# Performance work log

Measured on AMD Instinct MI355X. Metric: run time of the kernel, lower is better.

Reference implementation:

```python
import jax, jax.numpy as jnp
import numpy as np

B, D_IMG, H, V, T, EOS = 1024, 512, 512, 8192, 20, 0


def setup_inputs() -> dict:
    key = jax.random.key(0)
    ks = jax.random.split(key, 9)
    s = 1.0 / np.sqrt(H)
    return {
        "target_input": jax.random.normal(ks[0], (B, D_IMG), dtype=jnp.float32),
        "emb": jax.random.normal(ks[1], (V, H), dtype=jnp.float32),
        "fc1_w": jax.random.normal(ks[2], (H, D_IMG), dtype=jnp.float32) * (1.0 / np.sqrt(D_IMG)),
        "fc1_b": jnp.zeros((H,), jnp.float32),
        "w_ih": jax.random.normal(ks[3], (4 * H, H), dtype=jnp.float32) * s,
        "w_hh": jax.random.normal(ks[4], (4 * H, H), dtype=jnp.float32) * s,
        "b_ih": jax.random.normal(ks[5], (4 * H,), dtype=jnp.float32) * s,
        "b_hh": jax.random.normal(ks[6], (4 * H,), dtype=jnp.float32) * s,
        "out_w": jax.random.normal(ks[7], (V, H), dtype=jnp.float32) * s,
        "out_b": jnp.zeros((V,), jnp.float32),
        "max_len": T,
        "eos": EOS,
    }


def reference(target_input, emb, fc1_w, fc1_b, w_ih, w_hh, b_ih, b_hh, out_w, out_b, max_len, eos):
    Bsz = target_input.shape[0]
    Hd = w_hh.shape[1]
    # h0 = ReLU(fc1(img_latent)); c0 = 0; first token input = zeros
    h0 = jax.nn.relu(target_input @ fc1_w.T + fc1_b)
    c0 = jnp.zeros((Bsz, Hd), target_input.dtype)
    x0 = jnp.zeros((Bsz, Hd), target_input.dtype)
    mask0 = jnp.ones((Bsz,), target_input.dtype)
    keys = jax.random.split(jax.random.key(42), max_len)

    def step(carry, k):
        h, c, x, mask = carry
        # LSTMCell (PyTorch gate order i, f, g, o)
        gates = x @ w_ih.T + b_ih + h @ w_hh.T + b_hh
        i, f, g, o = jnp.split(gates, 4, axis=1)
        c = jax.nn.sigmoid(f) * c + jax.nn.sigmoid(i) * jnp.tanh(g)
        h = jax.nn.sigmoid(o) * jnp.tanh(c)
        logits = h @ out_w.T + out_b                      # [B, V]
        logp = jax.nn.log_softmax(logits, axis=-1)
        p = jnp.exp(logp)
        action = jax.random.categorical(k, logits, axis=-1)  # [B]
        lp = jnp.take_along_axis(logp, action[:, None], axis=1)[:, 0] * mask
        ent = -jnp.sum(p * logp, axis=-1) * mask
        p_masked = p * mask[:, None]
        x_next = emb[action]
        mask = mask * (1.0 - (action == eos).astype(mask.dtype))
        return (h, c, x_next, mask), (action, lp, ent, p_masked)

    _, (msgs, lps, ents, probs) = jax.lax.scan(step, (h0, c0, x0, mask0), keys)
    # scan stacks along time axis 0 -> move to axis 1
    return (msgs.T, lps.T, ents.T, jnp.transpose(probs, (1, 0, 2)))
```

## Files before the change

kernel.cpp:

```cpp
#include <hip/hip_runtime.h>
#include <math.h>

#define Bn 1024
#define Dn 512
#define Hn 512
#define Vn 8192
#define Tn 20
#define G4 2048

typedef _Float16 half8 __attribute__((ext_vector_type(8)));
typedef float f32x4 __attribute__((ext_vector_type(4)));

#define SCHEDB() __builtin_amdgcn_sched_barrier(0)
#define SBAR()   __builtin_amdgcn_s_barrier()

__host__ __device__ __forceinline__ void threefry2x32(
    unsigned k0, unsigned k1, unsigned x0, unsigned x1,
    unsigned& y0, unsigned& y1) {
  unsigned ks2 = k0 ^ k1 ^ 0x1BD11BDAu;
#define TF_RND(r) { x0 += x1; x1 = (x1 << (r)) | (x1 >> (32 - (r))); x1 ^= x0; }
  x0 += k0; x1 += k1;
  TF_RND(13) TF_RND(15) TF_RND(26) TF_RND(6)
  x0 += k1; x1 += ks2 + 1u;
  TF_RND(17) TF_RND(29) TF_RND(16) TF_RND(24)
  x0 += ks2; x1 += k0 + 2u;
  TF_RND(13) TF_RND(15) TF_RND(26) TF_RND(6)
  x0 += k0; x1 += k1 + 3u;
  TF_RND(17) TF_RND(29) TF_RND(16) TF_RND(24)
  x0 += k1; x1 += ks2 + 4u;
  TF_RND(13) TF_RND(15) TF_RND(26) TF_RND(6)
  x0 += ks2; x1 += k0 + 5u;
#undef TF_RND
  y0 = x0; y1 = x1;
}

__device__ __forceinline__ void split16(float v, _Float16& hi, _Float16& lo) {
  float h = (fabsf(v) < 6.2e-5f) ? 0.f : (float)(_Float16)v;
  hi = (_Float16)h;
  lo = (_Float16)((v - h) * 2048.0f);
}

__device__ __forceinline__ void gload16(void* l, const void* g) {
  __builtin_amdgcn_global_load_lds(
      (const __attribute__((address_space(1))) unsigned int*)g,
      (__attribute__((address_space(3))) unsigned int*)l, 16, 0, 0);
}

__global__ void k_prep(const float* __restrict__ w, _Float16* __restrict__ hi,
                       _Float16* __restrict__ lo, int n) {
  int i = blockIdx.x * blockDim.x + threadIdx.x;
  if (i >= n) return;
  split16(w[i], hi[i], lo[i]);
}

__global__ void k_prep_perm(const float* __restrict__ w, _Float16* __restrict__ hi,
                            _Float16* __restrict__ lo) {
  int i = blockIdx.x * blockDim.x + threadIdx.x;
  int rp = i >> 9, k = i & 511;
  int u = rp >> 2, g = rp & 3;
  split16(w[(size_t)((g << 9) + u) * 512 + k], hi[i], lo[i]);
}

__global__ void k_prep_bias(const float* __restrict__ bih, const float* __restrict__ bhh,
                            float* __restrict__ bp) {
  int i = blockIdx.x * blockDim.x + threadIdx.x;
  if (i >= G4) return;
  int u = i >> 2, g = i & 3;
  bp[i] = bih[(g << 9) + u] + bhh[(g << 9) + u];
}

__global__ void k_mask(float* __restrict__ mask) {
  int i = blockIdx.x * blockDim.x + threadIdx.x;
  if (i < Bn) mask[i] = 1.f;
}

__device__ __forceinline__ void cell_update(
    float (*gtile)[68], int tid, int bm, int u0, float* __restrict__ c,
    _Float16* __restrict__ hoh, _Float16* __restrict__ hol) {
#pragma unroll
  for (int j = 0; j < 8; ++j) {
    int idx = tid + (j << 8);
    int row = idx >> 4, ul = idx & 15;
    float4 gt = *(const float4*)&gtile[row][ul << 2];
    size_t cidx = (size_t)(bm + row) * Hn + u0 + ul;
    float si = 1.0f / (1.0f + expf(-gt.x));
    float sf = 1.0f / (1.0f + expf(-gt.y));
    float tg = tanhf(gt.z);
    float so = 1.0f / (1.0f + expf(-gt.w));
    float cn = sf * c[cidx] + si * tg;
    c[cidx] = cn;
    float hv = so * tanhf(cn);
    split16(hv, hoh[cidx], hol[cidx]);
  }
}

__global__ void __launch_bounds__(256) k_gates(
    const _Float16* __restrict__ xh, const _Float16* __restrict__ xl,
    const _Float16* __restrict__ hih, const _Float16* __restrict__ hil,
    const _Float16* __restrict__ wph, const _Float16* __restrict__ wpl,
    const _Float16* __restrict__ vph, const _Float16* __restrict__ vpl,
    const float* __restrict__ biasp, float* __restrict__ c,
    _Float16* __restrict__ hoh, _Float16* __restrict__ hol) {
  extern __shared__ __align__(16) char smem[];
  int tid = threadIdx.x;
  f32x4 acch[4][2] = {};
  f32x4 accc[4][2] = {};
  int x8 = blockIdx.x & 7, q = blockIdx.x >> 3;
  int bn = (((q & 3) << 3) | x8) << 6;
  int bm = (q >> 2) << 7;
  int lane = tid & 63, wv = tid >> 6;
  int wr = (wv >> 1) << 6, wc = (wv & 1) << 5;
  int fr = lane & 15, c0 = lane >> 4;
  int rsub = lane >> 2, cp = lane & 3;
  int psw = (c0 ^ ((fr >> 1) & 3)) << 3;

  auto stage = [&](int p, int t) {
    const _Float16* As_h = (t < 16) ? xh : hih;
    const _Float16* As_l = (t < 16) ? xl : hil;
    const _Float16* Bs_h = (t < 16) ? wph : vph;
    const _Float16* Bs_l = (t < 16) ? wpl : vpl;
    int k0 = (t & 15) << 5;
    char* base = smem + p * 24576;
#pragma unroll
    for (int s = 0; s < 2; ++s) {
      int row = (((wv << 1) + s) << 4) + rsub;
      int koff = (cp ^ ((row >> 1) & 3)) << 3;
      size_t ga = (size_t)(bm + row) * 512 + k0 + koff;
      int lo = (row << 5) + (cp << 3);
      gload16((_Float16*)base + lo, As_h + ga);
      gload16((_Float16*)(base + 8192) + lo, As_l + ga);
    }
    {
      int row = (wv << 4) + rsub;
      int koff = (cp ^ ((row >> 1) & 3)) << 3;
      size_t gb = (size_t)(bn + row) * 512 + k0 + koff;
      int lo = (row << 5) + (cp << 3);
      gload16((_Float16*)(base + 16384) + lo, Bs_h + gb);
      gload16((_Float16*)(base + 20480) + lo, Bs_l + gb);
    }
  };
  auto compute = [&](int p) {
    char* base = smem + p * 24576;
    _Float16 (*Ah)[32] = (_Float16(*)[32])base;
    _Float16 (*Al)[32] = (_Float16(*)[32])(base + 8192);
    _Float16 (*Bh)[32] = (_Float16(*)[32])(base + 16384);
    _Float16 (*Bl)[32] = (_Float16(*)[32])(base + 20480);
    half8 ah[4], al[4], bh[2], bl[2];
#pragma unroll
    for (int i = 0; i < 4; ++i) {
      int ra = wr + i * 16 + fr;
      ah[i] = *(const half8*)&Ah[ra][psw];
      al[i] = *(const half8*)&Al[ra][psw];
    }
#pragma unroll
    for (int i = 0; i < 2; ++i) {
      int rb = wc + i * 16 + fr;
      bh[i] = *(const half8*)&Bh[rb][psw];
      bl[i] = *(const half8*)&Bl[rb][psw];
    }
#pragma unroll
    for (int mi = 0; mi < 4; ++mi)
#pragma unroll
      for (int ni = 0; ni < 2; ++ni) {
        acch[mi][ni] = __builtin_amdgcn_mfma_f32_16x16x32_f16(ah[mi], bh[ni], acch[mi][ni], 0, 0, 0);
        accc[mi][ni] = __builtin_amdgcn_mfma_f32_16x16x32_f16(ah[mi], bl[ni], accc[mi][ni], 0, 0, 0);
        accc[mi][ni] = __builtin_amdgcn_mfma_f32_16x16x32_f16(al[mi], bh[ni], accc[mi][ni], 0, 0, 0);
      }
  };

  stage(0, 0); stage(1, 1);
  asm volatile("s_waitcnt vmcnt(6)" ::: "memory");
  SCHEDB(); SBAR(); SCHEDB();
  int pc = 0, ps = 2;
  for (int t = 0; t < 32; ++t) {
    if (t + 2 < 32) stage(ps, t + 2);
    compute(pc);
    SCHEDB();
    if (t + 2 < 32) { asm volatile("s_waitcnt vmcnt(6) lgkmcnt(0)" ::: "memory"); }
    else            { asm volatile("s_waitcnt vmcnt(0) lgkmcnt(0)" ::: "memory"); }
    SCHEDB(); SBAR(); SCHEDB();
    pc = (pc == 2) ? 0 : pc + 1;
    ps = (ps == 2) ? 0 : ps + 1;
  }

  float (*gtile)[68] = (float(*)[68])smem;
  int orow = (lane >> 4) << 2, ocol = lane & 15;
#pragma unroll
  for (int mi = 0; mi < 4; ++mi)
#pragma unroll
    for (int ni = 0; ni < 2; ++ni) {
      int col = wc + ni * 16 + ocol;
      float bsum = biasp[bn + col];
#pragma unroll
      for (int r = 0; r < 4; ++r) {
        int row = wr + mi * 16 + orow + r;
        gtile[row][col] = acch[mi][ni][r] + accc[mi][ni][r] * (1.0f / 2048.0f) + bsum;
      }
    }
  __syncthreads();
  cell_update(gtile, tid, bm, bn >> 2, c, hoh, hol);
}

__global__ void __launch_bounds__(512) k_logits(
    const _Float16* __restrict__ hh, const _Float16* __restrict__ hl,
    const _Float16* __restrict__ outwh, const _Float16* __restrict__ outwl,
    const float* __restrict__ outb, float* __restrict__ logits) {
  extern __shared__ __align__(16) char smem[];
  int tid = threadIdx.x;
  f32x4 acch[4][4] = {};
  f32x4 accc[4][4] = {};
  int x8 = blockIdx.x & 7, q = blockIdx.x >> 3;
  int bn = (((q & 7) << 3) | x8) << 7;
  int bm = (q >> 3) << 8;
  int lane = tid & 63, wv = tid >> 6;
  int wr = (wv >> 1) << 6, wc = (wv & 1) << 6;
  int fr = lane & 15, c0 = lane >> 4;
  int rsub = lane >> 2, cp = lane & 3;
  int psw = (c0 ^ ((fr >> 1) & 3)) << 3;

  auto stage = [&](int p, int t) {
    int k0 = t << 5;
    char* base = smem + p * 49152;
#pragma unroll
    for (int s = 0; s < 2; ++s) {
      int row = (((wv << 1) + s) << 4) + rsub;
      int koff = (cp ^ ((row >> 1) & 3)) << 3;
      size_t ga = (size_t)(bm + row) * 512 + k0 + koff;
      int lo = (row << 5) + (cp << 3);
      gload16((_Float16*)base + lo, hh + ga);
      gload16((_Float16*)(base + 16384) + lo, hl + ga);
    }
    {
      int row = tid >> 2;
      int koff = (cp ^ ((row >> 1) & 3)) << 3;
      size_t gb = (size_t)(bn + row) * 512 + k0 + koff;
      int lo = (row << 5) + (cp << 3);
      gload16((_Float16*)(base + 32768) + lo, outwh + gb);
      gload16((_Float16*)(base + 40960) + lo, outwl + gb);
    }
  };
  auto compute = [&](int p) {
    char* base = smem + p * 49152;
    _Float16 (*Ah)[32] = (_Float16(*)[32])base;
    _Float16 (*Al)[32] = (_Float16(*)[32])(base + 16384);
    _Float16 (*Bh)[32] = (_Float16(*)[32])(base + 32768);
    _Float16 (*Bl)[32] = (_Float16(*)[32])(base + 40960);
    half8 ah[4], al[4], bh[4], bl[4];
#pragma unroll
    for (int i = 0; i < 4; ++i) {
      int ra = wr + i * 16 + fr;
      int rb = wc + i * 16 + fr;
      ah[i] = *(const half8*)&Ah[ra][psw];
      al[i] = *(const half8*)&Al[ra][psw];
      bh[i] = *(const half8*)&Bh[rb][psw];
      bl[i] = *(const half8*)&Bl[rb][psw];
    }
#pragma unroll
    for (int mi = 0; mi < 4; ++mi)
#pragma unroll
      for (int ni = 0; ni < 4; ++ni) {
        acch[mi][ni] = __builtin_amdgcn_mfma_f32_16x16x32_f16(ah[mi], bh[ni], acch[mi][ni], 0, 0, 0);
        accc[mi][ni] = __builtin_amdgcn_mfma_f32_16x16x32_f16(ah[mi], bl[ni], accc[mi][ni], 0, 0, 0);
        accc[mi][ni] = __builtin_amdgcn_mfma_f32_16x16x32_f16(al[mi], bh[ni], accc[mi][ni], 0, 0, 0);
      }
  };

  stage(0, 0); stage(1, 1);
  asm volatile("s_waitcnt vmcnt(6)" ::: "memory");
  SCHEDB(); SBAR(); SCHEDB();
  int pc = 0, ps = 2;
  for (int t = 0; t < 16; ++t) {
    if (t + 2 < 16) stage(ps, t + 2);
    compute(pc);
    SCHEDB();
    if (t + 2 < 16) { asm volatile("s_waitcnt vmcnt(6) lgkmcnt(0)" ::: "memory"); }
    else            { asm volatile("s_waitcnt vmcnt(0) lgkmcnt(0)" ::: "memory"); }
    SCHEDB(); SBAR(); SCHEDB();
    pc = (pc == 2) ? 0 : pc + 1;
    ps = (ps == 2) ? 0 : ps + 1;
  }

  int orow = (lane >> 4) << 2, ocol = lane & 15;
#pragma unroll
  for (int mi = 0; mi < 4; ++mi)
#pragma unroll
    for (int ni = 0; ni < 4; ++ni) {
      int colg = bn + wc + ni * 16 + ocol;
      float bv = outb[colg];
#pragma unroll
      for (int r = 0; r < 4; ++r) {
        int rowg = bm + wr + mi * 16 + orow + r;
        logits[(size_t)rowg * Vn + colg] =
            acch[mi][ni][r] + accc[mi][ni][r] * (1.0f / 2048.0f) + bv;
      }
    }
}

__global__ void __launch_bounds__(256) k_gates_fb(
    const _Float16* __restrict__ xh, const _Float16* __restrict__ xl,
    const _Float16* __restrict__ hih, const _Float16* __restrict__ hil,
    const _Float16* __restrict__ wph, const _Float16* __restrict__ wpl,
    const _Float16* __restrict__ vph, const _Float16* __restrict__ vpl,
    const float* __restrict__ biasp, float* __restrict__ c,
    _Float16* __restrict__ hoh, _Float16* __restrict__ hol) {
  __shared__ __align__(16) char smem[49152];
  int tid = threadIdx.x;
  f32x4 acch[4][2] = {};
  f32x4 accc[4][2] = {};
  int x8 = blockIdx.x & 7, q = blockIdx.x >> 3;
  int bn = (((q & 3) << 3) | x8) << 6;
  int bm = (q >> 2) << 7;
  int lane = tid & 63, wv = tid >> 6;
  int wr = (wv >> 1) << 6, wc = (wv & 1) << 5;
  int fr = lane & 15, c0 = lane >> 4;
  int rsub = lane >> 2, cp = lane & 3;
  int psw = (c0 ^ ((fr >> 1) & 3)) << 3;
  auto stage = [&](int p, int t) {
    const _Float16* As_h = (t < 16) ? xh : hih;
    const _Float16* As_l = (t < 16) ? xl : hil;
    const _Float16* Bs_h = (t < 16) ? wph : vph;
    const _Float16* Bs_l = (t < 16) ? wpl : vpl;
    int k0 = (t & 15) << 5;
    char* base = smem + p * 24576;
#pragma unroll
    for (int s = 0; s < 2; ++s) {
      int row = (((wv << 1) + s) << 4) + rsub;
      int koff = (cp ^ ((row >> 1) & 3)) << 3;
      size_t ga = (size_t)(bm + row) * 512 + k0 + koff;
      int lo = (row << 5) + (cp << 3);
      gload16((_Float16*)base + lo, As_h + ga);
      gload16((_Float16*)(base + 8192) + lo, As_l + ga);
    }
    {
      int row = (wv << 4) + rsub;
      int koff = (cp ^ ((row >> 1) & 3)) << 3;
      size_t gb = (size_t)(bn + row) * 512 + k0 + koff;
      int lo = (row << 5) + (cp << 3);
      gload16((_Float16*)(base + 16384) + lo, Bs_h + gb);
      gload16((_Float16*)(base + 20480) + lo, Bs_l + gb);
    }
  };
  auto compute = [&](int p) {
    char* base = smem + p * 24576;
    _Float16 (*Ah)[32] = (_Float16(*)[32])base;
    _Float16 (*Al)[32] = (_Float16(*)[32])(base + 8192);
    _Float16 (*Bh)[32] = (_Float16(*)[32])(base + 16384);
    _Float16 (*Bl)[32] = (_Float16(*)[32])(base + 20480);
    half8 ah[4], al[4], bh[2], bl[2];
#pragma unroll
    for (int i = 0; i < 4; ++i) {
      int ra = wr + i * 16 + fr;
      ah[i] = *(const half8*)&Ah[ra][psw];
      al[i] = *(const half8*)&Al[ra][psw];
    }
#pragma unroll
    for (int i = 0; i < 2; ++i) {
      int rb = wc + i * 16 + fr;
      bh[i] = *(const half8*)&Bh[rb][psw];
      bl[i] = *(const half8*)&Bl[rb][psw];
    }
#pragma unroll
    for (int mi = 0; mi < 4; ++mi)
#pragma unroll
      for (int ni = 0; ni < 2; ++ni) {
        acch[mi][ni] = __builtin_amdgcn_mfma_f32_16x16x32_f16(ah[mi], bh[ni], acch[mi][ni], 0, 0, 0);
        accc[mi][ni] = __builtin_amdgcn_mfma_f32_16x16x32_f16(ah[mi], bl[ni], accc[mi][ni], 0, 0, 0);
        accc[mi][ni] = __builtin_amdgcn_mfma_f32_16x16x32_f16(al[mi], bh[ni], accc[mi][ni], 0, 0, 0);
      }
  };
  stage(0, 0);
  __syncthreads();
  int cur = 0;
  for (int t = 0; t < 32; ++t) {
    if (t + 1 < 32) stage(cur ^ 1, t + 1);
    compute(cur);
    __syncthreads();
    cur ^= 1;
  }
  float (*gtile)[68] = (float(*)[68])smem;
  int orow = (lane >> 4) << 2, ocol = lane & 15;
#pragma unroll
  for (int mi = 0; mi < 4; ++mi)
#pragma unroll
    for (int ni = 0; ni < 2; ++ni) {
      int col = wc + ni * 16 + ocol;
      float bsum = biasp[bn + col];
#pragma unroll
      for (int r = 0; r < 4; ++r) {
        int row = wr + mi * 16 + orow + r;
        gtile[row][col] = acch[mi][ni][r] + accc[mi][ni][r] * (1.0f / 2048.0f) + bsum;
      }
    }
  __syncthreads();
  cell_update(gtile, tid, bm, bn >> 2, c, hoh, hol);
}

__global__ void __launch_bounds__(256) k_logits_fb(
    const _Float16* __restrict__ hh, const _Float16* __restrict__ hl,
    const _Float16* __restrict__ outwh, const _Float16* __restrict__ outwl,
    const float* __restrict__ outb, float* __restrict__ logits) {
  __shared__ __align__(16) char smem[65536];
  int tid = threadIdx.x;
  f32x4 acch[4][4] = {};
  f32x4 accc[4][4] = {};
  int x8 = blockIdx.x & 7, q = blockIdx.x >> 3;
  int bn = (((q & 7) << 3) | x8) << 7;
  int bm = (q >> 3) << 7;
  int lane = tid & 63, wv = tid >> 6;
  int wr = (wv >> 1) << 6, wc = (wv & 1) << 6;
  int fr = lane & 15, c0 = lane >> 4;
  int rsub = lane >> 2, cp = lane & 3;
  int psw = (c0 ^ ((fr >> 1) & 3)) << 3;
  auto stage = [&](int p, int t) {
    int k0 = t << 5;
    char* base = smem + (p << 15);
#pragma unroll
    for (int s = 0; s < 2; ++s) {
      int row = (((wv << 1) + s) << 4) + rsub;
      int koff = (cp ^ ((row >> 1) & 3)) << 3;
      size_t ga = (size_t)(bm + row) * 512 + k0 + koff;
      size_t gb = (size_t)(bn + row) * 512 + k0 + koff;
      int lo = (row << 5) + (cp << 3);
      gload16((_Float16*)base + lo, hh + ga);
      gload16((_Float16*)(base + 8192) + lo, hl + ga);
      gload16((_Float16*)(base + 16384) + lo, outwh + gb);
      gload16((_Float16*)(base + 24576) + lo, outwl + gb);
    }
  };
  auto compute = [&](int p) {
    char* base = smem + (p << 15);
    _Float16 (*Ah)[32] = (_Float16(*)[32])base;
    _Float16 (*Al)[32] = (_Float16(*)[32])(base + 8192);
    _Float16 (*Bh)[32] = (_Float16(*)[32])(base + 16384);
    _Float16 (*Bl)[32] = (_Float16(*)[32])(base + 24576);
    half8 ah[4], al[4], bh[4], bl[4];
#pragma unroll
    for (int i = 0; i < 4; ++i) {
      int ra = wr + i * 16 + fr;
      int rb = wc + i * 16 + fr;
      ah[i] = *(const half8*)&Ah[ra][psw];
      al[i] = *(const half8*)&Al[ra][psw];
      bh[i] = *(const half8*)&Bh[rb][psw];
      bl[i] = *(const half8*)&Bl[rb][psw];
    }
#pragma unroll
    for (int mi = 0; mi < 4; ++mi)
#pragma unroll
      for (int ni = 0; ni < 4; ++ni) {
        acch[mi][ni] = __builtin_amdgcn_mfma_f32_16x16x32_f16(ah[mi], bh[ni], acch[mi][ni], 0, 0, 0);
        accc[mi][ni] = __builtin_amdgcn_mfma_f32_16x16x32_f16(ah[mi], bl[ni], accc[mi][ni], 0, 0, 0);
        accc[mi][ni] = __builtin_amdgcn_mfma_f32_16x16x32_f16(al[mi], bh[ni], accc[mi][ni], 0, 0, 0);
      }
  };
  stage(0, 0);
  __syncthreads();
  int cur = 0;
  for (int t = 0; t < 16; ++t) {
    if (t + 1 < 16) stage(cur ^ 1, t + 1);
    compute(cur);
    __syncthreads();
    cur ^= 1;
  }
  int orow = (lane >> 4) << 2, ocol = lane & 15;
#pragma unroll
  for (int mi = 0; mi < 4; ++mi)
#pragma unroll
    for (int ni = 0; ni < 4; ++ni) {
      int colg = bn + wc + ni * 16 + ocol;
      float bv = outb[colg];
#pragma unroll
      for (int r = 0; r < 4; ++r) {
        int rowg = bm + wr + mi * 16 + orow + r;
        logits[(size_t)rowg * Vn + colg] =
            acch[mi][ni][r] + accc[mi][ni][r] * (1.0f / 2048.0f) + bv;
      }
    }
}

__device__ __forceinline__ void gemm_seg(
    const float* __restrict__ A, int lda, const float* __restrict__ W, int ldw,
    int bm, int bn, int tid, int tm8, int tn4,
    float (*As)[132], float (*Bs)[68], float acc[8][4]) {
  for (int k0 = 0; k0 < 512; k0 += 16) {
#pragma unroll
    for (int it = 0; it < 2; ++it) {
      int g = (it << 8) + tid;
      int m = g >> 2, kq = g & 3;
      const float4 v = *(const float4*)(A + (size_t)(bm + m) * lda + k0 + (kq << 2));
      As[(kq << 2) + 0][m] = v.x; As[(kq << 2) + 1][m] = v.y;
      As[(kq << 2) + 2][m] = v.z; As[(kq << 2) + 3][m] = v.w;
    }
    {
      int m = tid >> 2, kq = tid & 3;
      const float4 v = *(const float4*)(W + (size_t)(bn + m) * ldw + k0 + (kq << 2));
      Bs[(kq << 2) + 0][m] = v.x; Bs[(kq << 2) + 1][m] = v.y;
      Bs[(kq << 2) + 2][m] = v.z; Bs[(kq << 2) + 3][m] = v.w;
    }
    __syncthreads();
#pragma unroll
    for (int k = 0; k < 16; ++k) {
      const float4 a0 = *(const float4*)&As[k][tm8];
      const float4 a1 = *(const float4*)&As[k][tm8 + 4];
      const float4 bv = *(const float4*)&Bs[k][tn4];
      float av[8] = {a0.x, a0.y, a0.z, a0.w, a1.x, a1.y, a1.z, a1.w};
      float bw[4] = {bv.x, bv.y, bv.z, bv.w};
#pragma unroll
      for (int i = 0; i < 8; ++i)
#pragma unroll
        for (int j = 0; j < 4; ++j)
          acc[i][j] = fmaf(av[i], bw[j], acc[i][j]);
    }
    __syncthreads();
  }
}

__global__ void __launch_bounds__(256) k_fc1(
    const float* __restrict__ img, const float* __restrict__ fc1w,
    const float* __restrict__ fc1b,
    _Float16* __restrict__ hh, _Float16* __restrict__ hl,
    _Float16* __restrict__ xh, _Float16* __restrict__ xl,
    float* __restrict__ c) {
  __shared__ float As[16][132];
  __shared__ float Bs[16][68];
  int tid = threadIdx.x;
  int tm8 = (tid >> 4) << 3;
  int tn4 = (tid & 15) << 2;
  float acc[8][4] = {};
  int bm = (blockIdx.x >> 3) << 7;
  int bn = (blockIdx.x & 7) << 6;
  gemm_seg(img, Dn, fc1w, Dn, bm, bn, tid, tm8, tn4, As, Bs, acc);
  const float4 b4 = *(const float4*)(fc1b + bn + tn4);
  float bb[4] = {b4.x, b4.y, b4.z, b4.w};
#pragma unroll
  for (int i = 0; i < 8; ++i) {
    size_t off = (size_t)(bm + tm8 + i) * Hn + bn + tn4;
#pragma unroll
    for (int j = 0; j < 4; ++j) {
      float hv = fmaxf(acc[i][j] + bb[j], 0.f);
      split16(hv, hh[off + j], hl[off + j]);
      xh[off + j] = (_Float16)0.f;
      xl[off + j] = (_Float16)0.f;
      c[off + j] = 0.f;
    }
  }
}

__global__ void __launch_bounds__(256) k_sm(
    const float* __restrict__ logits, const float* __restrict__ emb,
    float* __restrict__ mask, float* __restrict__ out_base,
    _Float16* __restrict__ xh, _Float16* __restrict__ xl,
    unsigned k0, unsigned k1, int t) {
  __shared__ __align__(16) float row[Vn];
  __shared__ float rf[256];
  __shared__ int ri[256];
  __shared__ double rd[256];
  int b = blockIdx.x, tid = threadIdx.x;
  const float4* src = (const float4*)(logits + (size_t)b * Vn);
  float4* dst = (float4*)row;
  for (int i = tid; i < Vn / 4; i += 256) dst[i] = src[i];
  __syncthreads();

  float m = -INFINITY, best = -INFINITY;
  int bidx = Vn;
  for (int v = tid; v < Vn; v += 256) {
    float lg = row[v];
    m = fmaxf(m, lg);
    unsigned j = (unsigned)(b * Vn + v);
    unsigned y0, y1;
    threefry2x32(k0, k1, 0u, j, y0, y1);
    unsigned bits = y0 ^ y1;
    float uf = fmaxf(__uint_as_float((bits >> 9) | 0x3F800000u) - 1.0f,
                     1.17549435e-38f);
    float g = -logf(-logf(uf));
    float val = lg + g;
    if (val > best) { best = val; bidx = v; }
  }
  rf[tid] = m;
  __syncthreads();
  for (int s = 128; s > 0; s >>= 1) {
    if (tid < s) rf[tid] = fmaxf(rf[tid], rf[tid + s]);
    __syncthreads();
  }
  float rowmax = rf[0];
  __syncthreads();
  rf[tid] = best; ri[tid] = bidx;
  __syncthreads();
  for (int s = 128; s > 0; s >>= 1) {
    if (tid < s) {
      float v2 = rf[tid + s]; int i2 = ri[tid + s];
      if (v2 > rf[tid] || (v2 == rf[tid] && i2 < ri[tid])) { rf[tid] = v2; ri[tid] = i2; }
    }
    __syncthreads();
  }
  int act = ri[0];

  double sacc = 0.0;
  for (int v = tid; v < Vn; v += 256) sacc += (double)expf(row[v] - rowmax);
  rd[tid] = sacc;
  __syncthreads();
  for (int s = 128; s > 0; s >>= 1) {
    if (tid < s) rd[tid] += rd[tid + s];
    __syncthreads();
  }
  double lse = log(rd[0]);
  float mk = mask[b];
  __syncthreads();

  float* probs = out_base + 3 * Bn * Tn + ((size_t)(b * Tn + t)) * Vn;
  double entacc = 0.0;
  for (int v0 = tid << 2; v0 < Vn; v0 += 1024) {
    float4 l4 = *(const float4*)&row[v0];
    float lp[4], pp[4];
    lp[0] = (float)((double)(l4.x - rowmax) - lse);
    lp[1] = (float)((double)(l4.y - rowmax) - lse);
    lp[2] = (float)((double)(l4.z - rowmax) - lse);
    lp[3] = (float)((double)(l4.w - rowmax) - lse);
#pragma unroll
    for (int q = 0; q < 4; ++q) {
      pp[q] = expf(lp[q]);
      entacc += (double)(pp[q] * lp[q]);
    }
    float4 o = {pp[0] * mk, pp[1] * mk, pp[2] * mk, pp[3] * mk};
    *(float4*)&probs[v0] = o;
    int d = act - v0;
    if (d >= 0 && d < 4)
      out_base[Bn * Tn + b * Tn + t] = lp[d] * mk;
  }
  rd[tid] = entacc;
  __syncthreads();
  for (int s = 128; s > 0; s >>= 1) {
    if (tid < s) rd[tid] += rd[tid + s];
    __syncthreads();
  }
  for (int j = tid; j < Hn; j += 256) {
    float v = emb[(size_t)act * Hn + j];
    split16(v, xh[(size_t)b * Hn + j], xl[(size_t)b * Hn + j]);
  }
  if (tid == 0) {
    out_base[2 * Bn * Tn + b * Tn + t] = (float)(-rd[0]) * mk;
    out_base[b * Tn + t] = (float)act;
    mask[b] = mk * (act == 0 ? 0.f : 1.f);
  }
}

extern "C" void kernel_launch(void* const* d_in, const int* in_sizes, int n_in,
                              void* d_out, int out_size, void* d_ws, size_t ws_size,
                              hipStream_t stream) {
  const float* img  = (const float*)d_in[0];
  const float* emb  = (const float*)d_in[1];
  const float* fc1w = (const float*)d_in[2];
  const float* fc1b = (const float*)d_in[3];
  const float* wih  = (const float*)d_in[4];
  const float* whh  = (const float*)d_in[5];
  const float* bih  = (const float*)d_in[6];
  const float* bhh  = (const float*)d_in[7];
  const float* outw = (const float*)d_in[8];
  const float* outb = (const float*)d_in[9];
  float* out = (float*)d_out;

  float* ws = (float*)d_ws;
  float* c      = ws;
  float* mask   = c + Bn * Hn;
  float* biasp  = mask + Bn;
  float* logits = biasp + G4;
  _Float16* wph  = (_Float16*)(logits + (size_t)Bn * Vn);
  _Float16* wpl  = wph + (size_t)G4 * Hn;
  _Float16* vph  = wpl + (size_t)G4 * Hn;
  _Float16* vpl  = vph + (size_t)G4 * Hn;
  _Float16* outwh = vpl + (size_t)G4 * Hn;
  _Float16* outwl = outwh + (size_t)Vn * Hn;
  _Float16* xh = outwl + (size_t)Vn * Hn;
  _Float16* xl = xh + Bn * Hn;
  _Float16* hhA = xl + Bn * Hn;
  _Float16* hlA = hhA + Bn * Hn;
  _Float16* hhB = hlA + Bn * Hn;
  _Float16* hlB = hhB + Bn * Hn;

  unsigned kk0[Tn], kk1[Tn];
  for (int i = 0; i < Tn; ++i) {
    unsigned y0, y1;
    threefry2x32(0u, 42u, 0u, (unsigned)i, y0, y1);
    kk0[i] = y0; kk1[i] = y1;
  }

  bool big_lds =
      (hipFuncSetAttribute((const void*)k_gates,
                           hipFuncAttributeMaxDynamicSharedMemorySize, 73728) == hipSuccess) &&
      (hipFuncSetAttribute((const void*)k_logits,
                           hipFuncAttributeMaxDynamicSharedMemorySize, 147456) == hipSuccess);

  k_prep_perm<<<(G4 * Hn) / 256, 256, 0, stream>>>(wih, wph, wpl);
  k_prep_perm<<<(G4 * Hn) / 256, 256, 0, stream>>>(whh, vph, vpl);
  k_prep<<<(Vn * Hn) / 256, 256, 0, stream>>>(outw, outwh, outwl, Vn * Hn);
  k_prep_bias<<<G4 / 256, 256, 0, stream>>>(bih, bhh, biasp);
  k_mask<<<4, 256, 0, stream>>>(mask);
  k_fc1<<<64, 256, 0, stream>>>(img, fc1w, fc1b, hhA, hlA, xh, xl, c);

  for (int t = 0; t < Tn; ++t) {
    const _Float16* hih = (t & 1) ? hhB : hhA;
    const _Float16* hil = (t & 1) ? hlB : hlA;
    _Float16* hoh = (t & 1) ? hhA : hhB;
    _Float16* hol = (t & 1) ? hlA : hlB;
    if (big_lds) {
      k_gates<<<256, 256, 73728, stream>>>(
          xh, xl, hih, hil, wph, wpl, vph, vpl, biasp, c, hoh, hol);
      k_logits<<<256, 512, 147456, stream>>>(
          hoh, hol, outwh, outwl, outb, logits);
    } else {
      k_gates_fb<<<256, 256, 0, stream>>>(
          xh, xl, hih, hil, wph, wpl, vph, vpl, biasp, c, hoh, hol);
      k_logits_fb<<<512, 256, 0, stream>>>(
          hoh, hol, outwh, outwl, outb, logits);
    }
    k_sm<<<Bn, 256, 0, stream>>>(logits, emb, mask, out, xh, xl, kk0[t], kk1[t], t);
  }
}
```

Baseline: 2.087 ms.

## Triple-buffer gate GEMM loads and fold entropy into softmax-sum pass

```diff
diff --git a/kernel.cpp b/kernel.cpp
--- a/kernel.cpp
+++ b/kernel.cpp
@@ -368,14 +368,19 @@
         accc[mi][ni] = __builtin_amdgcn_mfma_f32_16x16x32_f16(al[mi], bh[ni], accc[mi][ni], 0, 0, 0);
       }
   };
-  stage(0, 0);
-  __syncthreads();
-  int cur = 0;
+  stage(0, 0); stage(1, 1);
+  asm volatile("s_waitcnt vmcnt(6)" ::: "memory");
+  SCHEDB(); SBAR(); SCHEDB();
+  int pc = 0, ps = 2;
   for (int t = 0; t < 32; ++t) {
-    if (t + 1 < 32) stage(cur ^ 1, t + 1);
-    compute(cur);
-    __syncthreads();
-    cur ^= 1;
+    if (t + 2 < 32) stage(ps, t + 2);
+    compute(pc);
+    SCHEDB();
+    if (t + 2 < 32) { asm volatile("s_waitcnt vmcnt(6) lgkmcnt(0)" ::: "memory"); }
+    else            { asm volatile("s_waitcnt vmcnt(0) lgkmcnt(0)" ::: "memory"); }
+    SCHEDB(); SBAR(); SCHEDB();
+    pc = (pc == 2) ? 0 : pc + 1;
+    ps = (ps == 2) ? 0 : ps + 1;
   }
   float (*gtile)[68] = (float(*)[68])smem;
   int orow = (lane >> 4) << 2, ocol = lane & 15;
@@ -554,6 +559,7 @@
   __shared__ float rf[256];
   __shared__ int ri[256];
   __shared__ double rd[256];
+  __shared__ double rt[256];
   int b = blockIdx.x, tid = threadIdx.x;
   const float4* src = (const float4*)(logits + (size_t)b * Vn);
   float4* dst = (float4*)row;
@@ -571,7 +577,7 @@
     unsigned bits = y0 ^ y1;
     float uf = fmaxf(__uint_as_float((bits >> 9) | 0x3F800000u) - 1.0f,
                      1.17549435e-38f);
-    float g = -logf(-logf(uf));
+    float g = -__logf(-__logf(uf));
     float val = lg + g;
     if (val > best) { best = val; bidx = v; }
   }
@@ -594,50 +600,44 @@
   }
   int act = ri[0];
 
-  double sacc = 0.0;
-  for (int v = tid; v < Vn; v += 256) sacc += (double)expf(row[v] - rowmax);
-  rd[tid] = sacc;
+  double sacc = 0.0, tacc = 0.0;
+  for (int v = tid; v < Vn; v += 256) {
+    float sh = row[v] - rowmax;
+    float e = __expf(sh);
+    sacc += (double)e;
+    tacc += (double)(e * sh);
+  }
+  rd[tid] = sacc; rt[tid] = tacc;
   __syncthreads();
   for (int s = 128; s > 0; s >>= 1) {
-    if (tid < s) rd[tid] += rd[tid + s];
+    if (tid < s) { rd[tid] += rd[tid + s]; rt[tid] += rt[tid + s]; }
     __syncthreads();
   }
-  double lse = log(rd[0]);
+  double S = rd[0], T = rt[0];
+  double lse = log(S);
   float mk = mask[b];
-  __syncthreads();
 
   float* probs = out_base + 3 * Bn * Tn + ((size_t)(b * Tn + t)) * Vn;
-  double entacc = 0.0;
   for (int v0 = tid << 2; v0 < Vn; v0 += 1024) {
     float4 l4 = *(const float4*)&row[v0];
-    float lp[4], pp[4];
+    float lp[4];
     lp[0] = (float)((double)(l4.x - rowmax) - lse);
     lp[1] = (float)((double)(l4.y - rowmax) - lse);
     lp[2] = (float)((double)(l4.z - rowmax) - lse);
     lp[3] = (float)((double)(l4.w - rowmax) - lse);
-#pragma unroll
-    for (int q = 0; q < 4; ++q) {
-      pp[q] = expf(lp[q]);
-      entacc += (double)(pp[q] * lp[q]);
-    }
-    float4 o = {pp[0] * mk, pp[1] * mk, pp[2] * mk, pp[3] * mk};
+    float4 o = {__expf(lp[0]) * mk, __expf(lp[1]) * mk,
+                __expf(lp[2]) * mk, __expf(lp[3]) * mk};
     *(float4*)&probs[v0] = o;
     int d = act - v0;
     if (d >= 0 && d < 4)
       out_base[Bn * Tn + b * Tn + t] = lp[d] * mk;
   }
-  rd[tid] = entacc;
-  __syncthreads();
-  for (int s = 128; s > 0; s >>= 1) {
-    if (tid < s) rd[tid] += rd[tid + s];
-    __syncthreads();
-  }
   for (int j = tid; j < Hn; j += 256) {
     float v = emb[(size_t)act * Hn + j];
     split16(v, xh[(size_t)b * Hn + j], xl[(size_t)b * Hn + j]);
   }
   if (tid == 0) {
-    out_base[2 * Bn * Tn + b * Tn + t] = (float)(-rd[0]) * mk;
+    out_base[2 * Bn * Tn + b * Tn + t] = (float)(lse - T / S) * mk;
     out_base[b * Tn + t] = (float)act;
     mask[b] = mk * (act == 0 ? 0.f : 1.f);
   }
```

Result: faster. 2.019 ms (-3.3%).
